# Kernel tuning notes

Measured on AMD Instinct MI355X. Metric: run time of the kernel, lower is better.

The kernel has to match this reference:

```python
import jax, jax.numpy as jnp
import numpy as np

N, M, D_IN, H1, D, OUT_C = 2048, 128, 352, 512, 256, 13


def _lin_bn_relu(x, w, b, g, be):
    # 1x1 conv == linear over last dim; BN (eval) folded to per-channel affine (g, be)
    return jax.nn.relu(g * (x @ w.T + b) + be)


def _encode(x, wA, bA, gA, beA, wB, bB, gB, beB):
    return _lin_bn_relu(_lin_bn_relu(x, wA, bA, gA, beA), wB, bB, gB, beB)


def setup_inputs() -> dict:
    key = jax.random.key(0)
    ks = iter(jax.random.split(key, 64))

    def wgt(shape, s=0.05):
        return (jax.random.normal(next(ks), shape, jnp.float32) * s)

    def gamma(c):
        return 1.0 + 0.05 * jax.random.normal(next(ks), (c,), jnp.float32)

    inp = {}
    inp['ext_fea'] = jax.random.normal(next(ks), (N, D_IN), jnp.float32)
    inp['lab_fea'] = jax.random.normal(next(ks), (M, D_IN), jnp.float32)
    # convs1: 352->512->256, each Conv1d(1x1)+BN+ReLU
    inp.update(w1a=wgt((H1, D_IN)), b1a=wgt((H1,)), g1a=gamma(H1), be1a=wgt((H1,)))
    inp.update(w1b=wgt((D, H1)), b1b=wgt((D,)), g1b=gamma(D), be1b=wgt((D,)))
    # convs2: same shapes
    inp.update(w2a=wgt((H1, D_IN)), b2a=wgt((H1,)), g2a=gamma(H1), be2a=wgt((H1,)))
    inp.update(w2b=wgt((D, H1)), b2b=wgt((D,)), g2b=gamma(D), be2b=wgt((D,)))
    # wei_conv SharedMLP [256,32,64,256]: three Conv2d(1x1)+BN+ReLU
    inp.update(mw1=wgt((32, D)), mb1=wgt((32,)), mg1=gamma(32), mbe1=wgt((32,)))
    inp.update(mw2=wgt((64, 32)), mb2=wgt((64,)), mg2=gamma(64), mbe2=wgt((64,)))
    inp.update(mw3=wgt((D, 64)), mb3=wgt((D,)), mg3=gamma(D), mbe3=wgt((D,)))
    # fc
    inp.update(fcw=wgt((OUT_C, D)), fcb=wgt((OUT_C,)))
    return inp


def reference(ext_fea, lab_fea,
              w1a, b1a, g1a, be1a, w1b, b1b, g1b, be1b,
              w2a, b2a, g2a, be2a, w2b, b2b, g2b, be2b,
              mw1, mb1, mg1, mbe1, mw2, mb2, mg2, mbe2, mw3, mb3, mg3, mbe3,
              fcw, fcb):
    A = _encode(ext_fea, w1a, b1a, g1a, be1a, w1b, b1b, g1b, be1b)   # [N, 256]
    B = _encode(lab_fea, w2a, b2a, g2a, be2a, w2b, b2b, g2b, be2b)   # [M, 256]
    diff = A[:, None, :] - B[None, :, :]                             # [N, M, 256]
    h = _lin_bn_relu(diff, mw1, mb1, mg1, mbe1)                      # [N, M, 32]
    h = _lin_bn_relu(h, mw2, mb2, mg2, mbe2)                         # [N, M, 64]
    wei = _lin_bn_relu(h, mw3, mb3, mg3, mbe3)                       # [N, M, 256]
    # torch softmax over dim=-1 of [1,256,N,M] == over M == axis 1 here
    wei = jax.nn.softmax(wei, axis=1)
    att = jnp.sum(wei * diff, axis=1)                                # [N, 256]
    return att @ fcw.T + fcb                                         # [N, 13]
```

## Files before the change

kernel.cpp:

```cpp
#include <hip/hip_runtime.h>
#include <stdint.h>


typedef __attribute__((ext_vector_type(4))) float float4_t;
typedef __attribute__((ext_vector_type(4))) float f32x4;
typedef __attribute__((ext_vector_type(8))) short bf16x8;
typedef __attribute__((ext_vector_type(8))) unsigned short ushort8_t;
typedef __attribute__((ext_vector_type(4))) unsigned short ushort4_t;
typedef unsigned short ushort_t;

__device__ __forceinline__ float b2f(unsigned short u) {
  union { unsigned int i; float f; } v; v.i = ((unsigned int)u) << 16; return v.f;
}
__device__ __forceinline__ unsigned short f2b(float f) {
  union { float f; unsigned int i; } v; v.f = f;
  unsigned int x = v.i;
  return (unsigned short)((x + 0x7FFFu + ((x >> 16) & 1u)) >> 16);
}

template<int ISBF>
__device__ __forceinline__ ushort8_t ld8(const void* base, size_t idx) {
  if constexpr (ISBF) {
    return *(const ushort8_t*)((const ushort_t*)base + idx);
  } else {
    const float* p = (const float*)base + idx;
    float4_t v0 = *(const float4_t*)p;
    float4_t v1 = *(const float4_t*)(p + 4);
    ushort8_t u;
    #pragma unroll
    for (int e = 0; e < 4; ++e) { u[e] = f2b(v0[e]); u[4 + e] = f2b(v1[e]); }
    return u;
  }
}

template<int XBF, int WBF, int OUT_BF16>
__global__ __launch_bounds__(256) void enc_mfma(
    const void* __restrict__ XA, const void* __restrict__ WA,
    const float* __restrict__ bA, const float* __restrict__ gA, const float* __restrict__ beA,
    void* __restrict__ YA,
    const void* __restrict__ XB, const void* __restrict__ WB,
    const float* __restrict__ bB, const float* __restrict__ gB, const float* __restrict__ beB,
    void* __restrict__ YB, ushort_t* __restrict__ YBTb,
    int J, int K, int nbxA)
{
  __shared__ ushort_t Xs[2][32][40];
  __shared__ ushort_t Ws[2][32][40];
  const int bx = blockIdx.x, by = blockIdx.y;
  const void* X; const void* W;
  const float *bb, *gg, *bev; void* Y; int i0, isB;
  if (bx < nbxA) { X = XA; W = WA; bb = bA; gg = gA; bev = beA; Y = YA; i0 = bx * 32; isB = 0; }
  else           { X = XB; W = WB; bb = bB; gg = gB; bev = beB; Y = YB; i0 = (bx - nbxA) * 32; isB = 1; }
  const int j0 = by * 32;
  const int tid = threadIdx.x, w = tid >> 6, lane = tid & 63, lg = lane >> 4, lr = lane & 15;
  const int mt = w >> 1, ct = w & 1;
  const int row = tid >> 2, k8 = (tid & 3) * 8;

  f32x4 acc = f32x4{0.f, 0.f, 0.f, 0.f};

  ushort8_t sv = (row < 32) ? ld8<XBF>(X, (size_t)(i0 + row) * K + k8)
                            : ld8<WBF>(W, (size_t)(j0 + row - 32) * K + k8);
  for (int kt = 0; kt < K; kt += 32) {
    const int buf = (kt >> 5) & 1;
    if (row < 32) *(ushort8_t*)&Xs[buf][row][k8] = sv;
    else          *(ushort8_t*)&Ws[buf][row - 32][k8] = sv;
    __syncthreads();
    if (kt + 32 < K)
      sv = (row < 32) ? ld8<XBF>(X, (size_t)(i0 + row) * K + kt + 32 + k8)
                      : ld8<WBF>(W, (size_t)(j0 + row - 32) * K + kt + 32 + k8);
    bf16x8 af = *(const bf16x8*)&Xs[buf][mt * 16 + lr][lg * 8];
    bf16x8 bf_ = *(const bf16x8*)&Ws[buf][ct * 16 + lr][lg * 8];
    acc = __builtin_amdgcn_mfma_f32_16x16x32_bf16(af, bf_, acc, 0, 0, 0);
  }
  const int c = j0 + ct * 16 + lr;
  const float g = gg[c], bv = bb[c], ev = bev[c];
  #pragma unroll
  for (int r = 0; r < 4; ++r) {
    const int rowo = i0 + mt * 16 + 4 * lg + r;
    float t = fmaxf(g * (acc[r] + bv) + ev, 0.f);
    if (OUT_BF16) ((ushort_t*)Y)[(size_t)rowo * J + c] = f2b(t);
    else {
      ((float*)Y)[(size_t)rowo * J + c] = t;
      if (isB && YBTb) YBTb[(size_t)c * 128 + rowo] = f2b(t);
    }
  }
}

__global__ __launch_bounds__(256) void proj32(
    const float* __restrict__ Aenc, const float* __restrict__ Benc,
    const float* __restrict__ mw1, const float* __restrict__ mb1,
    const float* __restrict__ mg1, const float* __restrict__ mbe1,
    float* __restrict__ PA2, float* __restrict__ PB2, int nbxA,
    const float* __restrict__ mw2, const float* __restrict__ mw3,
    ushort_t* __restrict__ mw2b, ushort_t* __restrict__ mw3b)
{
  __shared__ float ps[4][32];
  const int tid = threadIdx.x, bx = blockIdx.x;
  if (bx >= nbxA + 32) {
    const int g = (bx - nbxA - 32) * 256 + tid;
    const float* s; ushort_t* d; int j;
    if (g < 256) { s = mw2; d = mw2b; j = g; }
    else         { s = mw3; d = mw3b; j = g - 256; }
    float4_t v0 = *(const float4_t*)&s[(size_t)j * 8];
    float4_t v1 = *(const float4_t*)&s[(size_t)j * 8 + 4];
    ushort8_t u;
    #pragma unroll
    for (int e = 0; e < 4; ++e) { u[e] = f2b(v0[e]); u[4 + e] = f2b(v1[e]); }
    *(ushort8_t*)&d[(size_t)j * 8] = u;
    return;
  }
  const float* X; float* P; int n0, wb;
  if (bx < nbxA) { X = Aenc; P = PA2; n0 = bx * 4; wb = 1; }
  else           { X = Benc; P = PB2; n0 = (bx - nbxA) * 4; wb = 0; }
  const int k = tid & 31, r = (tid >> 5) & 3, half = tid >> 7;
  const int n = n0 + r;
  const float* xp = &X[(size_t)n * 256 + half * 128];
  const float* wp = &mw1[k * 256 + half * 128];
  float s = 0.f;
  #pragma unroll 8
  for (int q = 0; q < 128; q += 4) {
    float4_t xv = *(const float4_t*)&xp[q];
    float4_t wv = *(const float4_t*)&wp[q];
    #pragma unroll
    for (int e = 0; e < 4; ++e) s = fmaf(xv[e], wv[e], s);
  }
  if (half == 1) ps[r][k] = s;
  __syncthreads();
  if (half == 0) {
    s += ps[r][k];
    P[(size_t)n * 32 + k] = wb ? (mg1[k] * (s + mb1[k]) + mbe1[k]) : (mg1[k] * s);
  }
}

__global__ __launch_bounds__(256, 2) void main_attn(
    const float* __restrict__ PA2, const float* __restrict__ PB2,
    const float* __restrict__ A, const ushort_t* __restrict__ BmTb,
    const ushort_t* __restrict__ mw2b, const float* __restrict__ mb2,
    const float* __restrict__ mg2, const float* __restrict__ mbe2,
    const ushort_t* __restrict__ mw3b, const float* __restrict__ mb3,
    const float* __restrict__ mg3, const float* __restrict__ mbe3,
    const float* __restrict__ fcw, const float* __restrict__ fcb,
    float* __restrict__ outp)
{
  __shared__ __align__(16) char smem[77824];
  const int tid = threadIdx.x;
  const int w = tid >> 6, lane = tid & 63, lg = lane >> 4, lr = lane & 15;
  const int n = blockIdx.x * 4 + w;
  ushort_t* h2s = (ushort_t*)(smem + w * 19456);
  float* attL   = (float*)(smem + w * 19456 + 18432);
  const float LOG2E = 1.4426950408889634f;

  {
    bf16x8 b1[4];
    float g2h[4], b2h[4], e2h[4];
    #pragma unroll
    for (int jt = 0; jt < 4; ++jt) {
      b1[jt] = *(const bf16x8*)&mw2b[(jt * 16 + lr) * 32 + lg * 8];
      const int j = jt * 16 + lr;
      g2h[jt] = mg2[j]; b2h[jt] = mb2[j]; e2h[jt] = mbe2[j];
    }
    const float* pa = &PA2[(size_t)n * 32 + lg * 8];
    float4_t pa0 = *(const float4_t*)pa;
    float4_t pa1 = *(const float4_t*)(pa + 4);
    #pragma unroll
    for (int mt = 0; mt < 8; ++mt) {
      const float* pb = &PB2[(size_t)(mt * 16 + lr) * 32 + lg * 8];
      float4_t pb0 = *(const float4_t*)pb;
      float4_t pb1 = *(const float4_t*)(pb + 4);
      bf16x8 a1;
      #pragma unroll
      for (int e = 0; e < 4; ++e) {
        a1[e]     = (short)f2b(fmaxf(pa0[e] - pb0[e], 0.f));
        a1[4 + e] = (short)f2b(fmaxf(pa1[e] - pb1[e], 0.f));
      }
      f32x4 acc1[4];
      #pragma unroll
      for (int jt = 0; jt < 4; ++jt) acc1[jt] = f32x4{0.f, 0.f, 0.f, 0.f};
      #pragma unroll
      for (int jt = 0; jt < 4; ++jt)
        acc1[jt] = __builtin_amdgcn_mfma_f32_16x16x32_bf16(a1, b1[jt], acc1[jt], 0, 0, 0);
      #pragma unroll
      for (int jt = 0; jt < 4; ++jt)
        #pragma unroll
        for (int r = 0; r < 4; ++r)
          h2s[(mt * 16 + 4 * lg + r) * 72 + jt * 16 + lr] =
              f2b(fmaxf(g2h[jt] * (acc1[jt][r] + b2h[jt]) + e2h[jt], 0.f));
    }
  }

  bf16x8 af0[8], af1[8];
  #pragma unroll
  for (int mt = 0; mt < 8; ++mt) {
    af0[mt] = *(const bf16x8*)&h2s[(mt * 16 + lr) * 72 + lg * 8];
    af1[mt] = *(const bf16x8*)&h2s[(mt * 16 + lr) * 72 + 32 + lg * 8];
  }

  #pragma unroll 4
  for (int ct = 0; ct < 16; ++ct) {
    const int c = ct * 16 + lr;
    bf16x8 bfr0 = *(const bf16x8*)&mw3b[(size_t)c * 64 + lg * 8];
    bf16x8 bfr1 = *(const bf16x8*)&mw3b[(size_t)c * 64 + 32 + lg * 8];
    f32x4 acc[8];
    #pragma unroll
    for (int mt = 0; mt < 8; ++mt) acc[mt] = f32x4{0.f, 0.f, 0.f, 0.f};
    #pragma unroll
    for (int mt = 0; mt < 8; ++mt) {
      acc[mt] = __builtin_amdgcn_mfma_f32_16x16x32_bf16(af0[mt], bfr0, acc[mt], 0, 0, 0);
      acc[mt] = __builtin_amdgcn_mfma_f32_16x16x32_bf16(af1[mt], bfr1, acc[mt], 0, 0, 0);
    }
    const float g = mg3[c];
    const float gs = g * LOG2E;
    const float cs = (g * mb3[c] + mbe3[c]) * LOG2E;
    f32x4 sm4 = f32x4{0.f, 0.f, 0.f, 0.f};
    f32x4 wb4 = f32x4{0.f, 0.f, 0.f, 0.f};
    #pragma unroll
    for (int mt = 0; mt < 8; ++mt) {
      ushort4_t bv4 = *(const ushort4_t*)&BmTb[(size_t)c * 128 + mt * 16 + 4 * lg];
      #pragma unroll
      for (int r = 0; r < 4; ++r) {
        float t = fmaf(gs, acc[mt][r], cs);
        float p = __builtin_amdgcn_exp2f(__builtin_amdgcn_fmed3f(t, 0.f, 80.f));
        sm4[r] += p;
        wb4[r] = fmaf(p, b2f(bv4[r]), wb4[r]);
      }
    }
    float sm = (sm4[0] + sm4[1]) + (sm4[2] + sm4[3]);
    float wb = (wb4[0] + wb4[1]) + (wb4[2] + wb4[3]);
    sm += __shfl_xor(sm, 16, 64);  wb += __shfl_xor(wb, 16, 64);
    sm += __shfl_xor(sm, 32, 64);  wb += __shfl_xor(wb, 32, 64);
    if (lg == 0)
      attL[c] = A[(size_t)n * 256 + c] - wb / sm;
  }

  {
    float4_t av = *(const float4_t*)&attL[lane * 4];
    #pragma unroll
    for (int o = 0; o < 13; ++o) {
      float4_t wv = *(const float4_t*)&fcw[(size_t)o * 256 + lane * 4];
      float s = av[0] * wv[0];
      s = fmaf(av[1], wv[1], s);
      s = fmaf(av[2], wv[2], s);
      s = fmaf(av[3], wv[3], s);
      #pragma unroll
      for (int st = 1; st <= 32; st <<= 1) s += __shfl_xor(s, st, 64);
      if (lane == 0) outp[(size_t)n * 13 + o] = s + fcb[o];
    }
  }
}

extern "C" void kernel_launch(void* const* d_in, const int* in_sizes, int n_in,
                              void* d_out, int out_size, void* d_ws, size_t ws_size,
                              hipStream_t stream)
{
  const float* ext = (const float*)d_in[0];
  const float* lab = (const float*)d_in[1];
  const float* w1a = (const float*)d_in[2];
  const float* b1a = (const float*)d_in[3];
  const float* g1a = (const float*)d_in[4];
  const float* be1a= (const float*)d_in[5];
  const float* w1b = (const float*)d_in[6];
  const float* b1b = (const float*)d_in[7];
  const float* g1b = (const float*)d_in[8];
  const float* be1b= (const float*)d_in[9];
  const float* w2a = (const float*)d_in[10];
  const float* b2a = (const float*)d_in[11];
  const float* g2a = (const float*)d_in[12];
  const float* be2a= (const float*)d_in[13];
  const float* w2b = (const float*)d_in[14];
  const float* b2b = (const float*)d_in[15];
  const float* g2b = (const float*)d_in[16];
  const float* be2b= (const float*)d_in[17];
  const float* mw1 = (const float*)d_in[18];
  const float* mb1 = (const float*)d_in[19];
  const float* mg1 = (const float*)d_in[20];
  const float* mbe1= (const float*)d_in[21];
  const float* mw2 = (const float*)d_in[22];
  const float* mb2 = (const float*)d_in[23];
  const float* mg2 = (const float*)d_in[24];
  const float* mbe2= (const float*)d_in[25];
  const float* mw3 = (const float*)d_in[26];
  const float* mb3 = (const float*)d_in[27];
  const float* mg3 = (const float*)d_in[28];
  const float* mbe3= (const float*)d_in[29];
  const float* fcw = (const float*)d_in[30];
  const float* fcb = (const float*)d_in[31];

  char* ws = (char*)d_ws;
  ushort_t* Y1ab = (ushort_t*)(ws);
  float*    PA2  = (float*)(ws);
  float*    PB2  = (float*)(ws + 262144);
  float*    Aenc = (float*)(ws + (2u << 20));
  char* b5 = ws + (4u << 20);
  ushort_t* mw2b  = (ushort_t*)(b5);
  ushort_t* mw3b  = (ushort_t*)(b5 + 4096);
  ushort_t* Y1bb  = (ushort_t*)(b5 + 36864);
  float*    Benc  = (float*)(b5 + 167936);
  ushort_t* BencTb= (ushort_t*)(b5 + 299008);

  enc_mfma<0, 0, 1><<<dim3(68, 16), 256, 0, stream>>>(
      (const void*)ext, (const void*)w1a, b1a, g1a, be1a, (void*)Y1ab,
      (const void*)lab, (const void*)w2a, b2a, g2a, be2a, (void*)Y1bb,
      (ushort_t*)nullptr, 512, 352, 64);
  enc_mfma<1, 0, 0><<<dim3(68, 8), 256, 0, stream>>>(
      (const void*)Y1ab, (const void*)w1b, b1b, g1b, be1b, (void*)Aenc,
      (const void*)Y1bb, (const void*)w2b, b2b, g2b, be2b, (void*)Benc,
      BencTb, 256, 512, 64);
  proj32<<<553, 256, 0, stream>>>(Aenc, Benc, mw1, mb1, mg1, mbe1, PA2, PB2, 512,
                                  mw2, mw3, mw2b, mw3b);
  main_attn<<<512, 256, 0, stream>>>(PA2, PB2, Aenc, BencTb,
                                     mw2b, mb2, mg2, mbe2, mw3b, mb3, mg3, mbe3,
                                     fcw, fcb, (float*)d_out);
}
```

Before: 86.09 us.

## Process M in two halves with fragment-major LDS layout to raise occupancy

Splits the 128-row M dimension into two 64-row halves and keeps running softmax-sum and weighted-sum accumulators in registers across the halves. This shrinks LDS per block from 76KB to 36KB and launch bounds request 3 blocks per CU. The h2 buffer is stored in an MFMA-fragment-major layout, and A fragments are read from LDS inside the channel loop instead of staying resident in registers. The BN affine is folded into a single fma. The cost is repeated mw3 loads and layer-3 setup per half plus extra LDS reads per channel tile, and tighter register limits may cause spills.

```diff
diff --git a/kernel.cpp b/kernel.cpp
--- a/kernel.cpp
+++ b/kernel.cpp
@@ -131,7 +131,7 @@
   }
 }
 
-__global__ __launch_bounds__(256, 2) void main_attn(
+__global__ __launch_bounds__(256, 3) void main_attn(
     const float* __restrict__ PA2, const float* __restrict__ PB2,
     const float* __restrict__ A, const ushort_t* __restrict__ BmTb,
     const ushort_t* __restrict__ mw2b, const float* __restrict__ mb2,
@@ -141,29 +141,37 @@
     const float* __restrict__ fcw, const float* __restrict__ fcb,
     float* __restrict__ outp)
 {
-  __shared__ __align__(16) char smem[77824];
+  __shared__ __align__(16) char smem[36864];
   const int tid = threadIdx.x;
   const int w = tid >> 6, lane = tid & 63, lg = lane >> 4, lr = lane & 15;
   const int n = blockIdx.x * 4 + w;
-  ushort_t* h2s = (ushort_t*)(smem + w * 19456);
-  float* attL   = (float*)(smem + w * 19456 + 18432);
+  ushort_t* h2f = (ushort_t*)(smem + w * 9216);
+  float* attL   = (float*)(smem + w * 9216 + 8192);
   const float LOG2E = 1.4426950408889634f;
 
-  {
-    bf16x8 b1[4];
-    float g2h[4], b2h[4], e2h[4];
-    #pragma unroll
-    for (int jt = 0; jt < 4; ++jt) {
-      b1[jt] = *(const bf16x8*)&mw2b[(jt * 16 + lr) * 32 + lg * 8];
-      const int j = jt * 16 + lr;
-      g2h[jt] = mg2[j]; b2h[jt] = mb2[j]; e2h[jt] = mbe2[j];
-    }
-    const float* pa = &PA2[(size_t)n * 32 + lg * 8];
-    float4_t pa0 = *(const float4_t*)pa;
-    float4_t pa1 = *(const float4_t*)(pa + 4);
-    #pragma unroll
-    for (int mt = 0; mt < 8; ++mt) {
-      const float* pb = &PB2[(size_t)(mt * 16 + lr) * 32 + lg * 8];
+  bf16x8 b1[4];
+  float g2h[4], c2h[4];
+  #pragma unroll
+  for (int jt = 0; jt < 4; ++jt) {
+    b1[jt] = *(const bf16x8*)&mw2b[(jt * 16 + lr) * 32 + lg * 8];
+    const int j = jt * 16 + lr;
+    const float g = mg2[j];
+    g2h[jt] = g; c2h[jt] = g * mb2[j] + mbe2[j];
+  }
+  const float* pa = &PA2[(size_t)n * 32 + lg * 8];
+  float4_t pa0 = *(const float4_t*)pa;
+  float4_t pa1 = *(const float4_t*)(pa + 4);
+
+  float smv[16], wbv[16];
+  #pragma unroll
+  for (int ct = 0; ct < 16; ++ct) { smv[ct] = 0.f; wbv[ct] = 0.f; }
+
+  #pragma unroll 1
+  for (int half = 0; half < 2; ++half) {
+    #pragma unroll
+    for (int mt = 0; mt < 4; ++mt) {
+      const int m = half * 64 + mt * 16 + lr;
+      const float* pb = &PB2[(size_t)m * 32 + lg * 8];
       float4_t pb0 = *(const float4_t*)pb;
       float4_t pb1 = *(const float4_t*)(pb + 4);
       bf16x8 a1;
@@ -179,56 +187,63 @@
       for (int jt = 0; jt < 4; ++jt)
         acc1[jt] = __builtin_amdgcn_mfma_f32_16x16x32_bf16(a1, b1[jt], acc1[jt], 0, 0, 0);
       #pragma unroll
-      for (int jt = 0; jt < 4; ++jt)
+      for (int jt = 0; jt < 4; ++jt) {
+        const int ks = jt >> 1;
+        const int lg_r = ((jt & 1) << 1) | (lr >> 3);
+        const int e = lr & 7;
+        const int base = (mt * 8 + ks * 4 + lg_r) * 128 + e;
         #pragma unroll
         for (int r = 0; r < 4; ++r)
-          h2s[(mt * 16 + 4 * lg + r) * 72 + jt * 16 + lr] =
-              f2b(fmaxf(g2h[jt] * (acc1[jt][r] + b2h[jt]) + e2h[jt], 0.f));
-    }
-  }
-
-  bf16x8 af0[8], af1[8];
+          h2f[base + (4 * lg + r) * 8] =
+              f2b(fmaxf(fmaf(g2h[jt], acc1[jt][r], c2h[jt]), 0.f));
+      }
+    }
+
+    #pragma unroll 4
+    for (int ct = 0; ct < 16; ++ct) {
+      const int c = ct * 16 + lr;
+      bf16x8 bfr0 = *(const bf16x8*)&mw3b[(size_t)c * 64 + lg * 8];
+      bf16x8 bfr1 = *(const bf16x8*)&mw3b[(size_t)c * 64 + 32 + lg * 8];
+      f32x4 acc[4];
+      #pragma unroll
+      for (int mt = 0; mt < 4; ++mt) acc[mt] = f32x4{0.f, 0.f, 0.f, 0.f};
+      #pragma unroll
+      for (int mt = 0; mt < 4; ++mt) {
+        bf16x8 af0 = *(const bf16x8*)&h2f[(mt * 8 + lg) * 128 + lr * 8];
+        acc[mt] = __builtin_amdgcn_mfma_f32_16x16x32_bf16(af0, bfr0, acc[mt], 0, 0, 0);
+        bf16x8 af1 = *(const bf16x8*)&h2f[(mt * 8 + 4 + lg) * 128 + lr * 8];
+        acc[mt] = __builtin_amdgcn_mfma_f32_16x16x32_bf16(af1, bfr1, acc[mt], 0, 0, 0);
+      }
+      const float g = mg3[c];
+      const float gs = g * LOG2E;
+      const float cs = (g * mb3[c] + mbe3[c]) * LOG2E;
+      f32x4 sm4 = f32x4{0.f, 0.f, 0.f, 0.f};
+      f32x4 wb4 = f32x4{0.f, 0.f, 0.f, 0.f};
+      #pragma unroll
+      for (int mt = 0; mt < 4; ++mt) {
+        ushort4_t bv4 = *(const ushort4_t*)&BmTb[(size_t)c * 128 + half * 64 + mt * 16 + 4 * lg];
+        #pragma unroll
+        for (int r = 0; r < 4; ++r) {
+          float t = fmaf(gs, acc[mt][r], cs);
+          float p = __builtin_amdgcn_exp2f(__builtin_amdgcn_fmed3f(t, 0.f, 80.f));
+          sm4[r] += p;
+          wb4[r] = fmaf(p, b2f(bv4[r]), wb4[r]);
+        }
+      }
+      smv[ct] += (sm4[0] + sm4[1]) + (sm4[2] + sm4[3]);
+      wbv[ct] += (wb4[0] + wb4[1]) + (wb4[2] + wb4[3]);
+    }
+  }
+
   #pragma unroll
-  for (int mt = 0; mt < 8; ++mt) {
-    af0[mt] = *(const bf16x8*)&h2s[(mt * 16 + lr) * 72 + lg * 8];
-    af1[mt] = *(const bf16x8*)&h2s[(mt * 16 + lr) * 72 + 32 + lg * 8];
-  }
-
-  #pragma unroll 4
   for (int ct = 0; ct < 16; ++ct) {
-    const int c = ct * 16 + lr;
-    bf16x8 bfr0 = *(const bf16x8*)&mw3b[(size_t)c * 64 + lg * 8];
-    bf16x8 bfr1 = *(const bf16x8*)&mw3b[(size_t)c * 64 + 32 + lg * 8];
-    f32x4 acc[8];
-    #pragma unroll
-    for (int mt = 0; mt < 8; ++mt) acc[mt] = f32x4{0.f, 0.f, 0.f, 0.f};
-    #pragma unroll
-    for (int mt = 0; mt < 8; ++mt) {
-      acc[mt] = __builtin_amdgcn_mfma_f32_16x16x32_bf16(af0[mt], bfr0, acc[mt], 0, 0, 0);
-      acc[mt] = __builtin_amdgcn_mfma_f32_16x16x32_bf16(af1[mt], bfr1, acc[mt], 0, 0, 0);
-    }
-    const float g = mg3[c];
-    const float gs = g * LOG2E;
-    const float cs = (g * mb3[c] + mbe3[c]) * LOG2E;
-    f32x4 sm4 = f32x4{0.f, 0.f, 0.f, 0.f};
-    f32x4 wb4 = f32x4{0.f, 0.f, 0.f, 0.f};
-    #pragma unroll
-    for (int mt = 0; mt < 8; ++mt) {
-      ushort4_t bv4 = *(const ushort4_t*)&BmTb[(size_t)c * 128 + mt * 16 + 4 * lg];
-      #pragma unroll
-      for (int r = 0; r < 4; ++r) {
-        float t = fmaf(gs, acc[mt][r], cs);
-        float p = __builtin_amdgcn_exp2f(__builtin_amdgcn_fmed3f(t, 0.f, 80.f));
-        sm4[r] += p;
-        wb4[r] = fmaf(p, b2f(bv4[r]), wb4[r]);
-      }
-    }
-    float sm = (sm4[0] + sm4[1]) + (sm4[2] + sm4[3]);
-    float wb = (wb4[0] + wb4[1]) + (wb4[2] + wb4[3]);
+    float sm = smv[ct], wb = wbv[ct];
     sm += __shfl_xor(sm, 16, 64);  wb += __shfl_xor(wb, 16, 64);
     sm += __shfl_xor(sm, 32, 64);  wb += __shfl_xor(wb, 32, 64);
-    if (lg == 0)
+    if (lg == 0) {
+      const int c = ct * 16 + lr;
       attL[c] = A[(size_t)n * 256 + c] - wb / sm;
+    }
   }
 
   {
```

New measurement: 96.30 us. 11.9% more time.
